# Kernel tuning notes

Measured on AMD Instinct MI355X. Metric: run time of the kernel, lower is better.

The kernel has to match this reference:

```python
import jax, jax.numpy as jnp
import numpy as np

GRID = 48          # static voxel-grid extent (positions generated in [0, GRID)^3)
K = 3              # kernel size per axis (odd -> offset = 0.0 in the original module)
C = (K - 1) // 2   # kernel center
VOXEL_SIZE = 1.0   # forward default in DeConvolution.call


def setup_inputs() -> dict:
    key = jax.random.key(0)
    k1, k2 = jax.random.split(key)
    g = np.arange(GRID)
    coords = np.stack(np.meshgrid(g, g, g, indexing='ij'), axis=-1).reshape(-1, 3)
    # sparse input point cloud: half-density sub-lattice; dense-ish output lattice
    inp_positions = jnp.asarray(coords[coords.sum(axis=1) % 2 == 0], jnp.float32)  # (55296, 3)
    out_positions = jnp.asarray(coords, jnp.float32)                               # (110592, 3)
    n_in = inp_positions.shape[0]
    cin, cout = 256, 256
    features = jax.random.normal(k1, (n_in, cin), dtype=jnp.float32)
    # SparseConvTranspose kernel: [k, k, k, in_channels, filters]
    W = jax.random.normal(k2, (K, K, K, cin, cout), dtype=jnp.float32) * 0.05
    return {"features": features, "inp_positions": inp_positions,
            "out_positions": out_positions, "W": W}


def reference(features, inp_positions, out_positions, W):
    # Voxelize. kernel is odd -> offset = 0.0, so v = floor(p / voxel_size).
    vin = jnp.floor(inp_positions / VOXEL_SIZE).astype(jnp.int32)   # (N_in, 3)
    vout = jnp.floor(out_positions / VOXEL_SIZE).astype(jnp.int32)  # (N_out, 3)
    n_in = features.shape[0]

    # Dense voxel -> input-row hash grid (-1 = empty voxel).
    grid = jnp.full((GRID, GRID, GRID), -1, dtype=jnp.int32)
    grid = grid.at[vin[:, 0], vin[:, 1], vin[:, 2]].set(
        jnp.arange(n_in, dtype=jnp.int32))

    out = jnp.zeros((vout.shape[0], W.shape[-1]), dtype=features.dtype)
    # Transposed sparse conv: out[j] += W[v_in - v_out + C] @ feat[i]
    # Static 27-tap loop; each tap is a gather + dense GEMM.
    for dx in range(-C, C + 1):
        for dy in range(-C, C + 1):
            for dz in range(-C, C + 1):
                u = vout + jnp.array([dx, dy, dz], dtype=jnp.int32)   # source voxel
                inb = jnp.all((u >= 0) & (u < GRID), axis=1)
                uc = jnp.clip(u, 0, GRID - 1)
                idx = grid[uc[:, 0], uc[:, 1], uc[:, 2]]              # (N_out,)
                valid = inb & (idx >= 0)
                g = jnp.where(valid[:, None],
                              features[jnp.maximum(idx, 0)], 0.0)     # (N_out, Cin)
                out = out + g @ W[dx + C, dy + C, dz + C]             # (N_out, Cout)
    return out
```

## Files before the change

### kernel.cpp

```cpp
#include <hip/hip_runtime.h>

#define NIN   55296
#define CIN   256
#define COUT  256
#define NTH   512
#define NBLK  432

typedef __attribute__((ext_vector_type(8))) _Float16 half8;
typedef __attribute__((ext_vector_type(4))) _Float16 half4;
typedef __attribute__((ext_vector_type(4))) float f32x4;

typedef const __attribute__((address_space(1))) void* gp_t;
typedef __attribute__((address_space(3))) void* lp_t;
__device__ __forceinline__ void gload16(const void* g, char* l) {
  __builtin_amdgcn_global_load_lds((gp_t)g, (lp_t)l, 16, 0, 0);
}

__global__ void k_feat_cvt(const float* __restrict__ f, _Float16* __restrict__ o, int n4) {
  int i = blockIdx.x * blockDim.x + threadIdx.x;
  if (i >= n4) return;
  f32x4 v = ((const f32x4*)f)[i];
  half4 r;
  r[0] = (_Float16)v[0]; r[1] = (_Float16)v[1];
  r[2] = (_Float16)v[2]; r[3] = (_Float16)v[3];
  ((half4*)o)[i] = r;
}

__global__ void k_w_cvt(const float* __restrict__ W, _Float16* __restrict__ Wt,
                        float* __restrict__ zeros) {
  int i = blockIdx.x * blockDim.x + threadIdx.x;
  int d   = i >> 16;
  int rem = i & 65535;
  int n   = rem >> 8;
  int k   = rem & 255;
  Wt[i] = (_Float16)W[(d << 16) + (k << 8) + n];
  if (blockIdx.x == 0 && threadIdx.x < 128) zeros[threadIdx.x] = 0.0f;
}

__global__ __launch_bounds__(NTH, 2)
void k_conv8(const _Float16* __restrict__ featb, const _Float16* __restrict__ wt,
             const char* __restrict__ zeros, float* __restrict__ out) {
  extern __shared__ char lds[];
  int* orow = (int*)(lds + 131072);

  const int braw = blockIdx.x;
  const int b    = (braw & 7) * 54 + (braw >> 3);
  const int p    = b & 1;
  const int tile = b >> 1;

  const int tid = threadIdx.x;
  const int w   = tid >> 6;
  const int l   = tid & 63;

  const int rr  = w * 16 + (l >> 2);
  const int swz = ((l & 3) ^ ((l >> 3) & 3)) * 16;

  int xs[2], ys[2], zs[2];
#pragma unroll
  for (int q = 0; q < 2; ++q) {
    int e = tile * 256 + q * 128 + rr;
    int c = e / 24;
    int zi = e - c * 24;
    int x = c / 48;
    int y = c - x * 48;
    xs[q] = x; ys[q] = y; zs[q] = 2 * zi + ((x + y + p) & 1);
  }
  const char* wtc   = (const char*)wt;
  const char* featc = (const char*)featb;
  const int bro0 = rr * 512 + swz;
  const int bro1 = (128 + rr) * 512 + swz;

  const int wm = w >> 2, wn = w & 3;
  const int lr = l & 15, kg = l >> 4;
  const int rsw = (kg ^ ((lr >> 1) & 3)) * 16;
  const int aRd = (wm * 128 + lr) * 64 + rsw;
  const int bRd = (wn * 64 + lr) * 64 + rsw;

  if (tid < 256) {
    int e = tile * 256 + tid;
    int c = e / 24;
    int zi = e - c * 24;
    int x = c / 48;
    int y = c - x * 48;
    int z = 2 * zi + ((x + y + p) & 1);
    orow[tid] = (x * 48 + y) * 48 + z;
  }

  const char* asrc[2];
  const char* wtile;
  auto setoff = [&](int d27) {
    int dx = d27 / 9 - 1, dy = (d27 / 3) % 3 - 1, dz = d27 % 3 - 1;
#pragma unroll
    for (int q = 0; q < 2; ++q) {
      int ux = xs[q] + dx, uy = ys[q] + dy, uz = zs[q] + dz;
      bool v = (unsigned)ux < 48u && (unsigned)uy < 48u && (unsigned)uz < 48u;
      int idx = (ux * 48 + uy) * 24 + (uz >> 1);
      asrc[q] = (v ? (featc + idx * 512) : zeros) + swz;
    }
    wtile = wtc + d27 * 131072;
  };

  int pn = p ? 0 : 1;
  setoff(pn);

  gload16(asrc[0],            lds + 0     + w * 1024);
  gload16(asrc[1],            lds + 8192  + w * 1024);
  gload16(asrc[0] + 64,       lds + 16384 + w * 1024);
  gload16(asrc[1] + 64,       lds + 24576 + w * 1024);
  gload16(wtile + bro0,       lds + 32768 + w * 1024);
  gload16(wtile + bro1,       lds + 40960 + w * 1024);
  gload16(wtile + bro0 + 64,  lds + 49152 + w * 1024);
  gload16(wtile + bro1 + 64,  lds + 57344 + w * 1024);

  f32x4 acc[8][4];
#pragma unroll
  for (int i = 0; i < 8; ++i)
#pragma unroll
    for (int j = 0; j < 4; ++j) acc[i][j] = (f32x4)0.0f;

  const int S = p ? 56 : 52;

  for (int s = 0; s < S; ++s) {
    __syncthreads();

    const char* Ab = lds + (s & 1) * 65536;

    half8 a0[8], a1[8], b0[4], b1[4];
#pragma unroll
    for (int nf = 0; nf < 4; ++nf) b0[nf] = *(const half8*)(Ab + 32768 + bRd + nf * 1024);
#pragma unroll
    for (int mf = 0; mf < 8; ++mf) a0[mf] = *(const half8*)(Ab + aRd + mf * 1024);
#pragma unroll
    for (int nf = 0; nf < 4; ++nf) b1[nf] = *(const half8*)(Ab + 49152 + bRd + nf * 1024);
#pragma unroll
    for (int mf = 0; mf < 8; ++mf) a1[mf] = *(const half8*)(Ab + 16384 + aRd + mf * 1024);

    const int sn = s + 1;
    if (sn < S) {
      if ((sn & 3) == 0) { pn += 2; setoff(pn); }
      char* Nb = lds + (sn & 1) * 65536;
      const int kb = (sn & 3) * 128;
      gload16(asrc[0] + kb,            Nb + 0     + w * 1024);
      gload16(asrc[1] + kb,            Nb + 8192  + w * 1024);
      gload16(asrc[0] + kb + 64,       Nb + 16384 + w * 1024);
      gload16(asrc[1] + kb + 64,       Nb + 24576 + w * 1024);
      gload16(wtile + bro0 + kb,       Nb + 32768 + w * 1024);
      gload16(wtile + bro1 + kb,       Nb + 40960 + w * 1024);
      gload16(wtile + bro0 + kb + 64,  Nb + 49152 + w * 1024);
      gload16(wtile + bro1 + kb + 64,  Nb + 57344 + w * 1024);
    }
    __builtin_amdgcn_sched_barrier(0);

    __builtin_amdgcn_s_setprio(1);
#pragma unroll
    for (int mf = 0; mf < 8; ++mf)
#pragma unroll
      for (int nf = 0; nf < 4; ++nf)
        acc[mf][nf] = __builtin_amdgcn_mfma_f32_16x16x32_f16(a0[mf], b0[nf], acc[mf][nf], 0, 0, 0);
#pragma unroll
    for (int mf = 0; mf < 8; ++mf)
#pragma unroll
      for (int nf = 0; nf < 4; ++nf)
        acc[mf][nf] = __builtin_amdgcn_mfma_f32_16x16x32_f16(a1[mf], b1[nf], acc[mf][nf], 0, 0, 0);
    __builtin_amdgcn_s_setprio(0);
  }

#pragma unroll
  for (int mf = 0; mf < 8; ++mf) {
#pragma unroll
    for (int i = 0; i < 4; ++i) {
      int r = wm * 128 + mf * 16 + kg * 4 + i;
      int o = orow[r];
      float* dst = out + (size_t)o * COUT + wn * 64 + lr;
#pragma unroll
      for (int nf = 0; nf < 4; ++nf) dst[nf * 16] = acc[mf][nf][i];
    }
  }
}

extern "C" void kernel_launch(void* const* d_in, const int* in_sizes, int n_in,
                              void* d_out, int out_size, void* d_ws, size_t ws_size,
                              hipStream_t stream) {
  const float* features = (const float*)d_in[0];
  const float* W = (const float*)d_in[3];
  float* out = (float*)d_out;

  char* ws = (char*)d_ws;
  _Float16* featb = (_Float16*)ws;
  _Float16* Wt    = (_Float16*)(ws + 28311552);
  float*    zeros = (float*)(ws + 28311552 + 3538944);

  (void)hipFuncSetAttribute(reinterpret_cast<const void*>(k_conv8),
                            hipFuncAttributeMaxDynamicSharedMemorySize, 132096);

  {
    int n4 = NIN * CIN / 4;
    k_feat_cvt<<<(n4 + 255) / 256, 256, 0, stream>>>(features, featb, n4);
  }
  k_w_cvt<<<27 * 65536 / 256, 256, 0, stream>>>(W, Wt, zeros);

  k_conv8<<<NBLK, NTH, 132096, stream>>>(featb, Wt, (const char*)zeros, out);
}
```

Before: 208.4 us.

## Load weight fragments straight to registers and stage only gathered features in LDS

The B (weight) operand is no longer staged through LDS. Each wave now loads its weight fragments directly from global memory into double-buffered registers, one step ahead. Only the gathered feature rows go through LDS, which halves shared memory per block, and the A fragments are read in two halves to cut register pressure. The goal is less LDS traffic and footprint, at the cost of more global loads per wave, since each weight fragment is fetched by both M-half wave groups, plus register double-buffering.

```diff
diff --git a/kernel.cpp b/kernel.cpp
--- a/kernel.cpp
+++ b/kernel.cpp
@@ -41,7 +41,7 @@
 void k_conv8(const _Float16* __restrict__ featb, const _Float16* __restrict__ wt,
              const char* __restrict__ zeros, float* __restrict__ out) {
   extern __shared__ char lds[];
-  int* orow = (int*)(lds + 131072);
+  int* orow = (int*)(lds + 65536);
 
   const int braw = blockIdx.x;
   const int b    = (braw & 7) * 54 + (braw >> 3);
@@ -52,29 +52,30 @@
   const int w   = tid >> 6;
   const int l   = tid & 63;
 
-  const int rr  = w * 16 + (l >> 2);
-  const int swz = ((l & 3) ^ ((l >> 3) & 3)) * 16;
-
-  int xs[2], ys[2], zs[2];
-#pragma unroll
-  for (int q = 0; q < 2; ++q) {
-    int e = tile * 256 + q * 128 + rr;
+  const int ks   = w >> 2;
+  const int w4   = w & 3;
+  const int swz  = ((l & 3) ^ ((l >> 3) & 3)) * 16;
+  const int stb  = ks * 16384 + w4 * 4096;
+  const int ks64 = ks * 64;
+
+  int xg[4], yg[4], zg[4];
+#pragma unroll
+  for (int g = 0; g < 4; ++g) {
+    int e = tile * 256 + w4 * 64 + g * 16 + (l >> 2);
     int c = e / 24;
     int zi = e - c * 24;
     int x = c / 48;
     int y = c - x * 48;
-    xs[q] = x; ys[q] = y; zs[q] = 2 * zi + ((x + y + p) & 1);
+    xg[g] = x; yg[g] = y; zg[g] = 2 * zi + ((x + y + p) & 1);
   }
   const char* wtc   = (const char*)wt;
   const char* featc = (const char*)featb;
-  const int bro0 = rr * 512 + swz;
-  const int bro1 = (128 + rr) * 512 + swz;
 
   const int wm = w >> 2, wn = w & 3;
   const int lr = l & 15, kg = l >> 4;
   const int rsw = (kg ^ ((lr >> 1) & 3)) * 16;
   const int aRd = (wm * 128 + lr) * 64 + rsw;
-  const int bRd = (wn * 64 + lr) * 64 + rsw;
+  const int bq  = (wn * 64 + lr) * 512 + kg * 16;
 
   if (tid < 256) {
     int e = tile * 256 + tid;
@@ -86,16 +87,16 @@
     orow[tid] = (x * 48 + y) * 48 + z;
   }
 
-  const char* asrc[2];
+  const char* asrc[4];
   const char* wtile;
   auto setoff = [&](int d27) {
     int dx = d27 / 9 - 1, dy = (d27 / 3) % 3 - 1, dz = d27 % 3 - 1;
 #pragma unroll
-    for (int q = 0; q < 2; ++q) {
-      int ux = xs[q] + dx, uy = ys[q] + dy, uz = zs[q] + dz;
+    for (int g = 0; g < 4; ++g) {
+      int ux = xg[g] + dx, uy = yg[g] + dy, uz = zg[g] + dz;
       bool v = (unsigned)ux < 48u && (unsigned)uy < 48u && (unsigned)uz < 48u;
       int idx = (ux * 48 + uy) * 24 + (uz >> 1);
-      asrc[q] = (v ? (featc + idx * 512) : zeros) + swz;
+      asrc[g] = (v ? (featc + idx * 512) : zeros) + swz + ks64;
     }
     wtile = wtc + d27 * 131072;
   };
@@ -103,14 +104,22 @@
   int pn = p ? 0 : 1;
   setoff(pn);
 
-  gload16(asrc[0],            lds + 0     + w * 1024);
-  gload16(asrc[1],            lds + 8192  + w * 1024);
-  gload16(asrc[0] + 64,       lds + 16384 + w * 1024);
-  gload16(asrc[1] + 64,       lds + 24576 + w * 1024);
-  gload16(wtile + bro0,       lds + 32768 + w * 1024);
-  gload16(wtile + bro1,       lds + 40960 + w * 1024);
-  gload16(wtile + bro0 + 64,  lds + 49152 + w * 1024);
-  gload16(wtile + bro1 + 64,  lds + 57344 + w * 1024);
+  {
+    char* Nb = lds + stb;
+    gload16(asrc[0], Nb);
+    gload16(asrc[1], Nb + 1024);
+    gload16(asrc[2], Nb + 2048);
+    gload16(asrc[3], Nb + 3072);
+  }
+  half8 bA[8], bB[8];
+  {
+    const char* wk = wtile + bq;
+#pragma unroll
+    for (int nf = 0; nf < 4; ++nf) {
+      bA[nf * 2 + 0] = *(const half8*)(wk + nf * 8192);
+      bA[nf * 2 + 1] = *(const half8*)(wk + nf * 8192 + 64);
+    }
+  }
 
   f32x4 acc[8][4];
 #pragma unroll
@@ -120,50 +129,56 @@
 
   const int S = p ? 56 : 52;
 
-  for (int s = 0; s < S; ++s) {
-    __syncthreads();
-
-    const char* Ab = lds + (s & 1) * 65536;
-
-    half8 a0[8], a1[8], b0[4], b1[4];
-#pragma unroll
-    for (int nf = 0; nf < 4; ++nf) b0[nf] = *(const half8*)(Ab + 32768 + bRd + nf * 1024);
-#pragma unroll
-    for (int mf = 0; mf < 8; ++mf) a0[mf] = *(const half8*)(Ab + aRd + mf * 1024);
-#pragma unroll
-    for (int nf = 0; nf < 4; ++nf) b1[nf] = *(const half8*)(Ab + 49152 + bRd + nf * 1024);
-#pragma unroll
-    for (int mf = 0; mf < 8; ++mf) a1[mf] = *(const half8*)(Ab + 16384 + aRd + mf * 1024);
-
-    const int sn = s + 1;
-    if (sn < S) {
-      if ((sn & 3) == 0) { pn += 2; setoff(pn); }
-      char* Nb = lds + (sn & 1) * 65536;
-      const int kb = (sn & 3) * 128;
-      gload16(asrc[0] + kb,            Nb + 0     + w * 1024);
-      gload16(asrc[1] + kb,            Nb + 8192  + w * 1024);
-      gload16(asrc[0] + kb + 64,       Nb + 16384 + w * 1024);
-      gload16(asrc[1] + kb + 64,       Nb + 24576 + w * 1024);
-      gload16(wtile + bro0 + kb,       Nb + 32768 + w * 1024);
-      gload16(wtile + bro1 + kb,       Nb + 40960 + w * 1024);
-      gload16(wtile + bro0 + kb + 64,  Nb + 49152 + w * 1024);
-      gload16(wtile + bro1 + kb + 64,  Nb + 57344 + w * 1024);
-    }
-    __builtin_amdgcn_sched_barrier(0);
-
-    __builtin_amdgcn_s_setprio(1);
-#pragma unroll
-    for (int mf = 0; mf < 8; ++mf)
-#pragma unroll
-      for (int nf = 0; nf < 4; ++nf)
-        acc[mf][nf] = __builtin_amdgcn_mfma_f32_16x16x32_f16(a0[mf], b0[nf], acc[mf][nf], 0, 0, 0);
-#pragma unroll
-    for (int mf = 0; mf < 8; ++mf)
-#pragma unroll
-      for (int nf = 0; nf < 4; ++nf)
-        acc[mf][nf] = __builtin_amdgcn_mfma_f32_16x16x32_f16(a1[mf], b1[nf], acc[mf][nf], 0, 0, 0);
-    __builtin_amdgcn_s_setprio(0);
-  }
+#define STEP(sv, HALF, BU, BP) do {                                                \
+    __syncthreads();                                                               \
+    const char* Ab = lds + (HALF);                                                 \
+    const int sn = (sv) + 1;                                                       \
+    if (sn < S) {                                                                  \
+      if ((sn & 3) == 0) { pn += 2; setoff(pn); }                                  \
+      const int kb = (sn & 3) * 128;                                               \
+      char* Nb = lds + ((HALF) ^ 32768) + stb;                                     \
+      gload16(asrc[0] + kb, Nb);                                                   \
+      gload16(asrc[1] + kb, Nb + 1024);                                            \
+      gload16(asrc[2] + kb, Nb + 2048);                                            \
+      gload16(asrc[3] + kb, Nb + 3072);                                            \
+      const char* wk = wtile + kb + bq;                                            \
+      _Pragma("unroll")                                                            \
+      for (int nf = 0; nf < 4; ++nf) {                                             \
+        BP[nf * 2 + 0] = *(const half8*)(wk + nf * 8192);                          \
+        BP[nf * 2 + 1] = *(const half8*)(wk + nf * 8192 + 64);                     \
+      }                                                                            \
+    }                                                                              \
+    half8 a[8];                                                                    \
+    _Pragma("unroll")                                                              \
+    for (int mf = 0; mf < 8; ++mf) a[mf] = *(const half8*)(Ab + aRd + mf * 1024);  \
+    __builtin_amdgcn_sched_barrier(0);                                             \
+    __builtin_amdgcn_s_setprio(1);                                                 \
+    _Pragma("unroll")                                                              \
+    for (int mf = 0; mf < 8; ++mf)                                                 \
+      _Pragma("unroll")                                                            \
+      for (int nf = 0; nf < 4; ++nf)                                               \
+        acc[mf][nf] = __builtin_amdgcn_mfma_f32_16x16x32_f16(                      \
+            a[mf], BU[nf * 2], acc[mf][nf], 0, 0, 0);                              \
+    __builtin_amdgcn_s_setprio(0);                                                 \
+    _Pragma("unroll")                                                              \
+    for (int mf = 0; mf < 8; ++mf)                                                 \
+      a[mf] = *(const half8*)(Ab + 16384 + aRd + mf * 1024);                       \
+    __builtin_amdgcn_sched_barrier(0);                                             \
+    __builtin_amdgcn_s_setprio(1);                                                 \
+    _Pragma("unroll")                                                              \
+    for (int mf = 0; mf < 8; ++mf)                                                 \
+      _Pragma("unroll")                                                            \
+      for (int nf = 0; nf < 4; ++nf)                                               \
+        acc[mf][nf] = __builtin_amdgcn_mfma_f32_16x16x32_f16(                      \
+            a[mf], BU[nf * 2 + 1], acc[mf][nf], 0, 0, 0);                          \
+    __builtin_amdgcn_s_setprio(0);                                                 \
+  } while (0)
+
+  for (int s2 = 0; s2 < S; s2 += 2) {
+    STEP(s2,     0,     bA, bB);
+    STEP(s2 + 1, 32768, bB, bA);
+  }
+#undef STEP
 
 #pragma unroll
   for (int mf = 0; mf < 8; ++mf) {
@@ -191,7 +206,7 @@
   float*    zeros = (float*)(ws + 28311552 + 3538944);
 
   (void)hipFuncSetAttribute(reinterpret_cast<const void*>(k_conv8),
-                            hipFuncAttributeMaxDynamicSharedMemorySize, 132096);
+                            hipFuncAttributeMaxDynamicSharedMemorySize, 66560);
 
   {
     int n4 = NIN * CIN / 4;
@@ -199,5 +214,5 @@
   }
   k_w_cvt<<<27 * 65536 / 256, 256, 0, stream>>>(W, Wt, zeros);
 
-  k_conv8<<<NBLK, NTH, 132096, stream>>>(featb, Wt, (const char*)zeros, out);
-}
+  k_conv8<<<NBLK, NTH, 66560, stream>>>(featb, Wt, (const char*)zeros, out);
+}
```

Result: slower. 647.4 us (+210.7%).

## Deepen conv pipeline to 4-stage LDS ring with half-size K steps

Applied to the files above, without the earlier changes.

The GEMM main loop changes from a double-buffered 64-wide K step per iteration to a 4-slot LDS ring of 32-wide K steps, prefetching two stages ahead. It replaces __syncthreads with explicit vmcnt waits plus s_barrier, so loads from the newest stage can stay in flight during compute. The LDS staging layout is also reorganised so each wave writes contiguous 2KB regions. The goal is to hide global-load latency better. In exchange there are twice as many barriers and iterations, and the hand-written waitcnt logic must stay correct.

```diff
diff --git a/kernel.cpp b/kernel.cpp
--- a/kernel.cpp
+++ b/kernel.cpp
@@ -52,29 +52,29 @@
   const int w   = tid >> 6;
   const int l   = tid & 63;
 
-  const int rr  = w * 16 + (l >> 2);
-  const int swz = ((l & 3) ^ ((l >> 3) & 3)) * 16;
+  const int swz  = ((l & 3) ^ ((l >> 3) & 3)) * 16;
+  const int stA0 = w * 2048;
 
   int xs[2], ys[2], zs[2];
 #pragma unroll
   for (int q = 0; q < 2; ++q) {
-    int e = tile * 256 + q * 128 + rr;
-    int c = e / 24;
+    int e  = tile * 256 + w * 32 + q * 16 + (l >> 2);
+    int c  = e / 24;
     int zi = e - c * 24;
-    int x = c / 48;
-    int y = c - x * 48;
+    int x  = c / 48;
+    int y  = c - x * 48;
     xs[q] = x; ys[q] = y; zs[q] = 2 * zi + ((x + y + p) & 1);
   }
   const char* wtc   = (const char*)wt;
   const char* featc = (const char*)featb;
-  const int bro0 = rr * 512 + swz;
-  const int bro1 = (128 + rr) * 512 + swz;
+  const int brow0 = (w * 32 + (l >> 2)) * 512 + swz;
+  const int brow1 = (w * 32 + 16 + (l >> 2)) * 512 + swz;
 
   const int wm = w >> 2, wn = w & 3;
   const int lr = l & 15, kg = l >> 4;
   const int rsw = (kg ^ ((lr >> 1) & 3)) * 16;
   const int aRd = (wm * 128 + lr) * 64 + rsw;
-  const int bRd = (wn * 64 + lr) * 64 + rsw;
+  const int bRd = 16384 + (wn * 64 + lr) * 64 + rsw;
 
   if (tid < 256) {
     int e = tile * 256 + tid;
@@ -85,6 +85,8 @@
     int z = 2 * zi + ((x + y + p) & 1);
     orow[tid] = (x * 48 + y) * 48 + z;
   }
+  asm volatile("s_waitcnt lgkmcnt(0)" ::: "memory");
+  __builtin_amdgcn_s_barrier();
 
   const char* asrc[2];
   const char* wtile;
@@ -100,17 +102,17 @@
     wtile = wtc + d27 * 131072;
   };
 
-  int pn = p ? 0 : 1;
-  setoff(pn);
+  const int pb = p ? 0 : 1;
+  setoff(pb);
 
-  gload16(asrc[0],            lds + 0     + w * 1024);
-  gload16(asrc[1],            lds + 8192  + w * 1024);
-  gload16(asrc[0] + 64,       lds + 16384 + w * 1024);
-  gload16(asrc[1] + 64,       lds + 24576 + w * 1024);
-  gload16(wtile + bro0,       lds + 32768 + w * 1024);
-  gload16(wtile + bro1,       lds + 40960 + w * 1024);
-  gload16(wtile + bro0 + 64,  lds + 49152 + w * 1024);
-  gload16(wtile + bro1 + 64,  lds + 57344 + w * 1024);
+  gload16(asrc[0],           lds + stA0);
+  gload16(asrc[1],           lds + stA0 + 1024);
+  gload16(wtile + brow0,     lds + 16384 + stA0);
+  gload16(wtile + brow1,     lds + 16384 + stA0 + 1024);
+  gload16(asrc[0] + 64,      lds + 32768 + stA0);
+  gload16(asrc[1] + 64,      lds + 32768 + stA0 + 1024);
+  gload16(wtile + brow0 + 64, lds + 32768 + 16384 + stA0);
+  gload16(wtile + brow1 + 64, lds + 32768 + 16384 + stA0 + 1024);
 
   f32x4 acc[8][4];
 #pragma unroll
@@ -118,50 +120,39 @@
 #pragma unroll
     for (int j = 0; j < 4; ++j) acc[i][j] = (f32x4)0.0f;
 
-  const int S = p ? 56 : 52;
+  const int S = p ? 112 : 104;
 
   for (int s = 0; s < S; ++s) {
-    __syncthreads();
+    if (s + 1 < S) asm volatile("s_waitcnt vmcnt(4)" ::: "memory");
+    else           asm volatile("s_waitcnt vmcnt(0)" ::: "memory");
+    __builtin_amdgcn_s_barrier();
+    __builtin_amdgcn_sched_barrier(0);
 
-    const char* Ab = lds + (s & 1) * 65536;
-
-    half8 a0[8], a1[8], b0[4], b1[4];
-#pragma unroll
-    for (int nf = 0; nf < 4; ++nf) b0[nf] = *(const half8*)(Ab + 32768 + bRd + nf * 1024);
-#pragma unroll
-    for (int mf = 0; mf < 8; ++mf) a0[mf] = *(const half8*)(Ab + aRd + mf * 1024);
-#pragma unroll
-    for (int nf = 0; nf < 4; ++nf) b1[nf] = *(const half8*)(Ab + 49152 + bRd + nf * 1024);
-#pragma unroll
-    for (int mf = 0; mf < 8; ++mf) a1[mf] = *(const half8*)(Ab + 16384 + aRd + mf * 1024);
-
-    const int sn = s + 1;
-    if (sn < S) {
-      if ((sn & 3) == 0) { pn += 2; setoff(pn); }
-      char* Nb = lds + (sn & 1) * 65536;
-      const int kb = (sn & 3) * 128;
-      gload16(asrc[0] + kb,            Nb + 0     + w * 1024);
-      gload16(asrc[1] + kb,            Nb + 8192  + w * 1024);
-      gload16(asrc[0] + kb + 64,       Nb + 16384 + w * 1024);
-      gload16(asrc[1] + kb + 64,       Nb + 24576 + w * 1024);
-      gload16(wtile + bro0 + kb,       Nb + 32768 + w * 1024);
-      gload16(wtile + bro1 + kb,       Nb + 40960 + w * 1024);
-      gload16(wtile + bro0 + kb + 64,  Nb + 49152 + w * 1024);
-      gload16(wtile + bro1 + kb + 64,  Nb + 57344 + w * 1024);
+    const int s2 = s + 2;
+    if (s2 < S) {
+      if ((s2 & 7) == 0) setoff(pb + ((s2 >> 3) << 1));
+      const int kb = (s2 & 7) * 64;
+      char* Nb = lds + (s2 & 3) * 32768;
+      gload16(asrc[0] + kb,           Nb + stA0);
+      gload16(asrc[1] + kb,           Nb + stA0 + 1024);
+      gload16(wtile + brow0 + kb,     Nb + 16384 + stA0);
+      gload16(wtile + brow1 + kb,     Nb + 16384 + stA0 + 1024);
     }
     __builtin_amdgcn_sched_barrier(0);
+
+    const char* Ab = lds + (s & 3) * 32768;
+    half8 a[8], bf[4];
+#pragma unroll
+    for (int nf = 0; nf < 4; ++nf) bf[nf] = *(const half8*)(Ab + bRd + nf * 1024);
+#pragma unroll
+    for (int mf = 0; mf < 8; ++mf) a[mf] = *(const half8*)(Ab + aRd + mf * 1024);
 
     __builtin_amdgcn_s_setprio(1);
 #pragma unroll
     for (int mf = 0; mf < 8; ++mf)
 #pragma unroll
       for (int nf = 0; nf < 4; ++nf)
-        acc[mf][nf] = __builtin_amdgcn_mfma_f32_16x16x32_f16(a0[mf], b0[nf], acc[mf][nf], 0, 0, 0);
-#pragma unroll
-    for (int mf = 0; mf < 8; ++mf)
-#pragma unroll
-      for (int nf = 0; nf < 4; ++nf)
-        acc[mf][nf] = __builtin_amdgcn_mfma_f32_16x16x32_f16(a1[mf], b1[nf], acc[mf][nf], 0, 0, 0);
+        acc[mf][nf] = __builtin_amdgcn_mfma_f32_16x16x32_f16(a[mf], bf[nf], acc[mf][nf], 0, 0, 0);
     __builtin_amdgcn_s_setprio(0);
   }
 
```

Measured after the change: 225.3 us. 1.08x slower.

## Deepen LDS pipeline: triple-buffer A, double-buffer B with vmcnt waits

Applied to the files above, without the earlier changes.

The shared-memory staging is restructured so the gathered feature (A) tiles are triple-buffered and prefetched two K-steps ahead, while the weight (B) tiles are double-buffered one step ahead. The blanket __syncthreads is replaced by explicit s_waitcnt vmcnt plus s_barrier, so loads for later stages can stay in flight across iterations. This aims to hide the latency of the irregular gathers behind MFMA work. The output-row LDS table is dropped in favour of recomputing row indices in the epilogue. LDS use rises to 160 KB, and the prologue contains a redundant extra weight load.

```diff
diff --git a/kernel.cpp b/kernel.cpp
--- a/kernel.cpp
+++ b/kernel.cpp
@@ -41,7 +41,7 @@
 void k_conv8(const _Float16* __restrict__ featb, const _Float16* __restrict__ wt,
              const char* __restrict__ zeros, float* __restrict__ out) {
   extern __shared__ char lds[];
-  int* orow = (int*)(lds + 131072);
+  char* ldsB = lds + 98304;
 
   const int braw = blockIdx.x;
   const int b    = (braw & 7) * 54 + (braw >> 3);
@@ -76,19 +76,8 @@
   const int aRd = (wm * 128 + lr) * 64 + rsw;
   const int bRd = (wn * 64 + lr) * 64 + rsw;
 
-  if (tid < 256) {
-    int e = tile * 256 + tid;
-    int c = e / 24;
-    int zi = e - c * 24;
-    int x = c / 48;
-    int y = c - x * 48;
-    int z = 2 * zi + ((x + y + p) & 1);
-    orow[tid] = (x * 48 + y) * 48 + z;
-  }
-
   const char* asrc[2];
-  const char* wtile;
-  auto setoff = [&](int d27) {
+  auto setoffA = [&](int d27) {
     int dx = d27 / 9 - 1, dy = (d27 / 3) % 3 - 1, dz = d27 % 3 - 1;
 #pragma unroll
     for (int q = 0; q < 2; ++q) {
@@ -97,20 +86,37 @@
       int idx = (ux * 48 + uy) * 24 + (uz >> 1);
       asrc[q] = (v ? (featc + idx * 512) : zeros) + swz;
     }
-    wtile = wtc + d27 * 131072;
   };
 
-  int pn = p ? 0 : 1;
-  setoff(pn);
-
-  gload16(asrc[0],            lds + 0     + w * 1024);
-  gload16(asrc[1],            lds + 8192  + w * 1024);
-  gload16(asrc[0] + 64,       lds + 16384 + w * 1024);
-  gload16(asrc[1] + 64,       lds + 24576 + w * 1024);
-  gload16(wtile + bro0,       lds + 32768 + w * 1024);
-  gload16(wtile + bro1,       lds + 40960 + w * 1024);
-  gload16(wtile + bro0 + 64,  lds + 49152 + w * 1024);
-  gload16(wtile + bro1 + 64,  lds + 57344 + w * 1024);
+  const int pb = p ? 0 : 1;
+  const char* wtileB = wtc + pb * 131072;
+  setoffA(pb);
+
+  gload16(wtileB + bro0,      ldsB + 16384 + w * 1024);
+  ;
+  {
+    char* Bb = ldsB;
+    gload16(wtileB + bro0,      Bb + 0     + w * 1024);
+    gload16(wtileB + bro1,      Bb + 8192  + w * 1024);
+    gload16(wtileB + bro0 + 64, Bb + 16384 + w * 1024);
+    gload16(wtileB + bro1 + 64, Bb + 24576 + w * 1024);
+  }
+  __builtin_amdgcn_sched_barrier(0);
+  {
+    char* Ab = lds;
+    gload16(asrc[0],      Ab + 0     + w * 1024);
+    gload16(asrc[1],      Ab + 8192  + w * 1024);
+    gload16(asrc[0] + 64, Ab + 16384 + w * 1024);
+    gload16(asrc[1] + 64, Ab + 24576 + w * 1024);
+  }
+  __builtin_amdgcn_sched_barrier(0);
+  {
+    char* Ab = lds + 32768;
+    gload16(asrc[0] + 128, Ab + 0     + w * 1024);
+    gload16(asrc[1] + 128, Ab + 8192  + w * 1024);
+    gload16(asrc[0] + 192, Ab + 16384 + w * 1024);
+    gload16(asrc[1] + 192, Ab + 24576 + w * 1024);
+  }
 
   f32x4 acc[8][4];
 #pragma unroll
@@ -121,34 +127,49 @@
   const int S = p ? 56 : 52;
 
   for (int s = 0; s < S; ++s) {
-    __syncthreads();
-
-    const char* Ab = lds + (s & 1) * 65536;
+    if (s + 2 < S) asm volatile("s_waitcnt vmcnt(4)" ::: "memory");
+    else           asm volatile("s_waitcnt vmcnt(0)" ::: "memory");
+    __builtin_amdgcn_s_barrier();
+    __builtin_amdgcn_sched_barrier(0);
+
+    const int sB = s + 1;
+    if (sB < S) {
+      if ((sB & 3) == 0) wtileB = wtc + (pb + ((sB >> 2) << 1)) * 131072;
+      const int kb = (sB & 3) * 128;
+      char* Bb = ldsB + (sB & 1) * 32768;
+      gload16(wtileB + bro0 + kb,      Bb + 0     + w * 1024);
+      gload16(wtileB + bro1 + kb,      Bb + 8192  + w * 1024);
+      gload16(wtileB + bro0 + kb + 64, Bb + 16384 + w * 1024);
+      gload16(wtileB + bro1 + kb + 64, Bb + 24576 + w * 1024);
+    }
+    __builtin_amdgcn_sched_barrier(0);
+
+    const int sA = s + 2;
+    if (sA < S) {
+      if ((sA & 3) == 0) setoffA(pb + ((sA >> 2) << 1));
+      const int kb = (sA & 3) * 128;
+      int ia = sA - (sA / 3) * 3;
+      char* Ab = lds + ia * 32768;
+      gload16(asrc[0] + kb,      Ab + 0     + w * 1024);
+      gload16(asrc[1] + kb,      Ab + 8192  + w * 1024);
+      gload16(asrc[0] + kb + 64, Ab + 16384 + w * 1024);
+      gload16(asrc[1] + kb + 64, Ab + 24576 + w * 1024);
+    }
+    __builtin_amdgcn_sched_barrier(0);
+
+    const int ic = s - (s / 3) * 3;
+    const char* Ab = lds + ic * 32768;
+    const char* Bb = ldsB + (s & 1) * 32768;
 
     half8 a0[8], a1[8], b0[4], b1[4];
 #pragma unroll
-    for (int nf = 0; nf < 4; ++nf) b0[nf] = *(const half8*)(Ab + 32768 + bRd + nf * 1024);
+    for (int nf = 0; nf < 4; ++nf) b0[nf] = *(const half8*)(Bb + bRd + nf * 1024);
 #pragma unroll
     for (int mf = 0; mf < 8; ++mf) a0[mf] = *(const half8*)(Ab + aRd + mf * 1024);
 #pragma unroll
-    for (int nf = 0; nf < 4; ++nf) b1[nf] = *(const half8*)(Ab + 49152 + bRd + nf * 1024);
+    for (int nf = 0; nf < 4; ++nf) b1[nf] = *(const half8*)(Bb + 16384 + bRd + nf * 1024);
 #pragma unroll
     for (int mf = 0; mf < 8; ++mf) a1[mf] = *(const half8*)(Ab + 16384 + aRd + mf * 1024);
-
-    const int sn = s + 1;
-    if (sn < S) {
-      if ((sn & 3) == 0) { pn += 2; setoff(pn); }
-      char* Nb = lds + (sn & 1) * 65536;
-      const int kb = (sn & 3) * 128;
-      gload16(asrc[0] + kb,            Nb + 0     + w * 1024);
-      gload16(asrc[1] + kb,            Nb + 8192  + w * 1024);
-      gload16(asrc[0] + kb + 64,       Nb + 16384 + w * 1024);
-      gload16(asrc[1] + kb + 64,       Nb + 24576 + w * 1024);
-      gload16(wtile + bro0 + kb,       Nb + 32768 + w * 1024);
-      gload16(wtile + bro1 + kb,       Nb + 40960 + w * 1024);
-      gload16(wtile + bro0 + kb + 64,  Nb + 49152 + w * 1024);
-      gload16(wtile + bro1 + kb + 64,  Nb + 57344 + w * 1024);
-    }
     __builtin_amdgcn_sched_barrier(0);
 
     __builtin_amdgcn_s_setprio(1);
@@ -170,7 +191,12 @@
 #pragma unroll
     for (int i = 0; i < 4; ++i) {
       int r = wm * 128 + mf * 16 + kg * 4 + i;
-      int o = orow[r];
+      int e = tile * 256 + r;
+      int c = e / 24;
+      int zi = e - c * 24;
+      int x = c / 48;
+      int y = c - x * 48;
+      int o = c * 48 + 2 * zi + ((x + y + p) & 1);
       float* dst = out + (size_t)o * COUT + wn * 64 + lr;
 #pragma unroll
       for (int nf = 0; nf < 4; ++nf) dst[nf * 16] = acc[mf][nf][i];
@@ -191,7 +217,7 @@
   float*    zeros = (float*)(ws + 28311552 + 3538944);
 
   (void)hipFuncSetAttribute(reinterpret_cast<const void*>(k_conv8),
-                            hipFuncAttributeMaxDynamicSharedMemorySize, 132096);
+                            hipFuncAttributeMaxDynamicSharedMemorySize, 163840);
 
   {
     int n4 = NIN * CIN / 4;
@@ -199,5 +225,5 @@
   }
   k_w_cvt<<<27 * 65536 / 256, 256, 0, stream>>>(W, Wt, zeros);
 
-  k_conv8<<<NBLK, NTH, 132096, stream>>>(featb, Wt, (const char*)zeros, out);
-}
+  k_conv8<<<NBLK, NTH, 163840, stream>>>(featb, Wt, (const char*)zeros, out);
+}
```

Result: slower. 219.6 us (+5.4%).
